# Performance work log

Hardware: AMD Instinct MI355X
Metric: run time of the kernel (lower is better)

The kernel has to match this reference:

```python
import jax, jax.numpy as jnp
import numpy as np

NUM_LAYERS = 2
H = 8        # num_head
D = 64       # dim_head
HID = H * D  # hidden_size = 512
FF = 2048    # dim_ff
SLEN = 256
BSZ = 16
IN_DIM = 512


def setup_inputs() -> dict:
    key = jax.random.key(0)
    ks = jax.random.split(key, 12)
    std = 1.0 / np.sqrt(D)
    return {
        'x': jax.random.normal(ks[0], (SLEN, BSZ, IN_DIM), jnp.float32),
        'in_w': jax.random.normal(ks[1], (IN_DIM, HID), jnp.float32) * 0.02,
        'in_b': jnp.zeros((HID,), jnp.float32),
        'Wy': jax.random.normal(ks[2], (NUM_LAYERS, H, D, D), jnp.float32) * std,
        'Wq': jax.random.normal(ks[3], (NUM_LAYERS, H, D, D), jnp.float32) * std,
        'Wk': jax.random.normal(ks[4], (NUM_LAYERS, H, D, D), jnp.float32) * std,
        'wb': jax.random.normal(ks[5], (NUM_LAYERS, H, D, 4), jnp.float32) * std,
        'Wout': jax.random.normal(ks[6], (NUM_LAYERS, HID, HID), jnp.float32) * 0.02,
        'ln_g': jnp.ones((NUM_LAYERS, HID), jnp.float32),
        'ln_b': jnp.zeros((NUM_LAYERS, HID), jnp.float32),
        'ff_w1': jax.random.normal(ks[7], (NUM_LAYERS, HID, FF), jnp.float32) * 0.02,
        'ff_b1': jnp.zeros((NUM_LAYERS, FF), jnp.float32),
        'ff_w2': jax.random.normal(ks[8], (NUM_LAYERS, FF, HID), jnp.float32) * 0.02,
        'ff_b2': jnp.zeros((NUM_LAYERS, HID), jnp.float32),
        'core_state': 0,
    }


def _layer_norm(x, g, b):
    m = jnp.mean(x, axis=-1, keepdims=True)
    v = jnp.mean(jnp.square(x - m), axis=-1, keepdims=True)
    return (x - m) / jnp.sqrt(v + 1e-5) * g + b


def _sr_block(h, Wy0, Wq0, Wk0, wb0, Wout_l):
    # h: [L, B, HID]. Self-referential fast-weight recurrence (self_ref_v0).
    L, B, _ = h.shape
    x = jax.nn.softmax(h.reshape(L, B, H, D), axis=-1)  # [L,B,H,D]
    init = (
        jnp.broadcast_to(Wy0, (B, H, D, D)),
        jnp.broadcast_to(Wq0, (B, H, D, D)),
        jnp.broadcast_to(Wk0, (B, H, D, D)),
        jnp.broadcast_to(wb0, (B, H, D, 4)),
    )

    def step(carry, xt):
        Wy_, Wq_, Wk_, wb_ = carry
        y = jnp.einsum('bhij,bhj->bhi', Wy_, xt)
        q = jax.nn.softmax(jnp.einsum('bhij,bhj->bhi', Wq_, xt), axis=-1)
        k = jax.nn.softmax(jnp.einsum('bhij,bhj->bhi', Wk_, xt), axis=-1)
        beta = jax.nn.sigmoid(jnp.einsum('bhjf,bhj->bhf', wb_, xt))  # [B,H,4]
        d = q - k
        dy = jnp.einsum('bhij,bhj->bhi', Wy_, d)  # W(q) - W(k) by linearity
        dq = jnp.einsum('bhij,bhj->bhi', Wq_, d)
        dk = jnp.einsum('bhij,bhj->bhi', Wk_, d)
        db = jnp.einsum('bhjf,bhj->bhf', wb_, d)  # [B,H,4]
        kT = k[..., None, :]  # [B,H,1,D]
        Wy_n = Wy_ + beta[..., 0:1, None] * dy[..., :, None] * kT
        Wq_n = Wq_ + beta[..., 1:2, None] * dq[..., :, None] * kT
        Wk_n = Wk_ + beta[..., 2:3, None] * dk[..., :, None] * kT
        wb_n = wb_ + beta[..., 3][..., None, None] * k[..., :, None] * db[..., None, :]
        return (Wy_n, Wq_n, Wk_n, wb_n), y

    _, ys = jax.lax.scan(step, init, x)            # ys: [L,B,H,D]
    out = ys.reshape(L, B, H * D) @ Wout_l          # out_linear (no bias)
    return h + out


def reference(x, in_w, in_b, Wy, Wq, Wk, wb, Wout, ln_g, ln_b,
              ff_w1, ff_b1, ff_w2, ff_b2, core_state):
    out = x @ in_w + in_b  # input_proj
    for i in range(NUM_LAYERS):
        out = _sr_block(out, Wy[i], Wq[i], Wk[i], wb[i], Wout[i])
        y = _layer_norm(out, ln_g[i], ln_b[i])
        out = out + (jax.nn.relu(y @ ff_w1[i] + ff_b1[i]) @ ff_w2[i] + ff_b2[i])
    return out
```

## Files before the change

kernel.cpp:

```cpp
#include <hip/hip_runtime.h>
#include <hip/hip_bf16.h>
#include <math.h>

#define SLEN 256
#define BSZ  16
#define NH   8
#define HD   64
#define HID  512
#define FFD  2048
#define MROWS (SLEN*BSZ)

typedef __attribute__((ext_vector_type(8))) short short8v;
typedef __attribute__((ext_vector_type(4))) float float4v;
typedef unsigned short ushort_t;

#define SYNC_LDS() do { \
  asm volatile("s_waitcnt lgkmcnt(0)" ::: "memory"); \
  __builtin_amdgcn_s_barrier(); \
} while (0)

template<int C> __device__ __forceinline__ float dppf(float x){
  return __int_as_float(__builtin_amdgcn_update_dpp(__float_as_int(x), __float_as_int(x), C, 0xF, 0xF, false));
}

__device__ __forceinline__ float rsum64(float v){
  v += dppf<0xB1>(v);
  v += dppf<0x4E>(v);
  v += dppf<0x141>(v);
  v += dppf<0x140>(v);
  v += __int_as_float(__builtin_amdgcn_update_dpp(0, __float_as_int(v), 0x142, 0xa, 0xF, false));
  v += __int_as_float(__builtin_amdgcn_update_dpp(0, __float_as_int(v), 0x143, 0xc, 0xF, false));
  return __int_as_float(__builtin_amdgcn_readlane(__float_as_int(v), 63));
}

__device__ __forceinline__ float rmax64(float v){
  v = fmaxf(v, dppf<0xB1>(v));
  v = fmaxf(v, dppf<0x4E>(v));
  v = fmaxf(v, dppf<0x141>(v));
  v = fmaxf(v, dppf<0x140>(v));
  v = fmaxf(v, __int_as_float(__builtin_amdgcn_update_dpp((int)0xff800000u, __float_as_int(v), 0x142, 0xa, 0xF, false)));
  v = fmaxf(v, __int_as_float(__builtin_amdgcn_update_dpp((int)0xff800000u, __float_as_int(v), 0x143, 0xc, 0xF, false)));
  return __int_as_float(__builtin_amdgcn_readlane(__float_as_int(v), 63));
}

__device__ __forceinline__ void split_bf16(float f, ushort_t& h, ushort_t& l){
  unsigned u = __float_as_uint(f);
  unsigned r = u + (0x7fffu + ((u >> 16) & 1u));
  h = (ushort_t)(r >> 16);
  float hf = __uint_as_float(((unsigned)h) << 16);
  float lo = f - hf;
  unsigned u2 = __float_as_uint(lo);
  unsigned r2 = u2 + (0x7fffu + ((u2 >> 16) & 1u));
  l = (ushort_t)(r2 >> 16);
}

template<int N, int K, bool BIAS, bool RESID, bool RELU>
__global__ __launch_bounds__(512) void gemm_mfma(
    const float* __restrict__ A, const float* __restrict__ B,
    const float* __restrict__ bias, const float* __restrict__ resid,
    float* __restrict__ C)
{
  __shared__ ushort_t Ah[128][40];
  __shared__ ushort_t Al[128][40];
  __shared__ ushort_t Bh[128][40];
  __shared__ ushort_t Bl[128][40];

  const int tid = threadIdx.x;
  const int wv = tid >> 6, lane = tid & 63;
  const int wm = wv >> 2, wn = wv & 3;
  const int l15 = lane & 15, l16 = lane >> 4;
  const int row0 = blockIdx.y * 128, col0 = blockIdx.x * 128;

  const int sar = tid >> 2, sak = (tid & 3) * 8;
  const int sbc = tid & 127, sbk = (tid >> 7) * 8;

  float4v acc[4][2];
#pragma unroll
  for (int i = 0; i < 4; ++i)
#pragma unroll
    for (int n = 0; n < 2; ++n) acc[i][n] = (float4v)(0.f);

  for (int k0 = 0; k0 < K; k0 += 32) {
    {
      const float* ap = &A[(size_t)(row0 + sar) * K + k0 + sak];
      float4 a0 = *reinterpret_cast<const float4*>(ap);
      float4 a1 = *reinterpret_cast<const float4*>(ap + 4);
      float av[8] = {a0.x, a0.y, a0.z, a0.w, a1.x, a1.y, a1.z, a1.w};
      short8v vh, vl;
#pragma unroll
      for (int j = 0; j < 8; ++j) {
        ushort_t h, l; split_bf16(av[j], h, l);
        vh[j] = (short)h; vl[j] = (short)l;
      }
      *reinterpret_cast<short8v*>(&Ah[sar][sak]) = vh;
      *reinterpret_cast<short8v*>(&Al[sar][sak]) = vl;
    }
    {
      float bv[8];
#pragma unroll
      for (int j = 0; j < 8; ++j)
        bv[j] = B[(size_t)(k0 + sbk + j) * N + col0 + sbc];
      short8v vh, vl;
#pragma unroll
      for (int j = 0; j < 8; ++j) {
        ushort_t h, l; split_bf16(bv[j], h, l);
        vh[j] = (short)h; vl[j] = (short)l;
      }
      *reinterpret_cast<short8v*>(&Bh[sbc][sbk]) = vh;
      *reinterpret_cast<short8v*>(&Bl[sbc][sbk]) = vl;
    }
    __syncthreads();

    short8v ah[4], al[4], bh[2], bl[2];
#pragma unroll
    for (int i = 0; i < 4; ++i) {
      const int r = wm * 64 + i * 16 + l15;
      ah[i] = *reinterpret_cast<const short8v*>(&Ah[r][l16 * 8]);
      al[i] = *reinterpret_cast<const short8v*>(&Al[r][l16 * 8]);
    }
#pragma unroll
    for (int n = 0; n < 2; ++n) {
      const int c = wn * 32 + n * 16 + l15;
      bh[n] = *reinterpret_cast<const short8v*>(&Bh[c][l16 * 8]);
      bl[n] = *reinterpret_cast<const short8v*>(&Bl[c][l16 * 8]);
    }
#pragma unroll
    for (int i = 0; i < 4; ++i)
#pragma unroll
      for (int n = 0; n < 2; ++n) {
        acc[i][n] = __builtin_amdgcn_mfma_f32_16x16x32_bf16(ah[i], bh[n], acc[i][n], 0, 0, 0);
        acc[i][n] = __builtin_amdgcn_mfma_f32_16x16x32_bf16(ah[i], bl[n], acc[i][n], 0, 0, 0);
        acc[i][n] = __builtin_amdgcn_mfma_f32_16x16x32_bf16(al[i], bh[n], acc[i][n], 0, 0, 0);
      }
    __syncthreads();
  }

#pragma unroll
  for (int i = 0; i < 4; ++i) {
#pragma unroll
    for (int n = 0; n < 2; ++n) {
      const int col = col0 + wn * 32 + n * 16 + l15;
      float bs = BIAS ? bias[col] : 0.f;
#pragma unroll
      for (int r = 0; r < 4; ++r) {
        const int row = row0 + wm * 64 + i * 16 + l16 * 4 + r;
        float v = acc[i][n][r] + bs;
        if (RESID) v += resid[(size_t)row * N + col];
        if (RELU)  v = fmaxf(v, 0.f);
        C[(size_t)row * N + col] = v;
      }
    }
  }
}

__global__ __launch_bounds__(64) void layernorm_k(
    const float* __restrict__ in, const float* __restrict__ g,
    const float* __restrict__ b, float* __restrict__ out)
{
  const int row = blockIdx.x, lane = threadIdx.x;
  const float* p = in + (size_t)row * HID + lane * 8;
  float4 v0 = *reinterpret_cast<const float4*>(p);
  float4 v1 = *reinterpret_cast<const float4*>(p + 4);
  float s = v0.x + v0.y + v0.z + v0.w + v1.x + v1.y + v1.z + v1.w;
  s = rsum64(s);
  const float mean = s * (1.0f / HID);
  float x[8] = {v0.x, v0.y, v0.z, v0.w, v1.x, v1.y, v1.z, v1.w};
  float sq = 0.f;
#pragma unroll
  for (int j = 0; j < 8; ++j) { float d = x[j] - mean; sq += d * d; }
  sq = rsum64(sq);
  const float rstd = rsqrtf(sq * (1.0f / HID) + 1e-5f);
  float4 g0 = *reinterpret_cast<const float4*>(&g[lane * 8]);
  float4 g1 = *reinterpret_cast<const float4*>(&g[lane * 8 + 4]);
  float4 b0 = *reinterpret_cast<const float4*>(&b[lane * 8]);
  float4 b1 = *reinterpret_cast<const float4*>(&b[lane * 8 + 4]);
  float gg[8] = {g0.x, g0.y, g0.z, g0.w, g1.x, g1.y, g1.z, g1.w};
  float bb[8] = {b0.x, b0.y, b0.z, b0.w, b1.x, b1.y, b1.z, b1.w};
  float o[8];
#pragma unroll
  for (int j = 0; j < 8; ++j) o[j] = (x[j] - mean) * rstd * gg[j] + bb[j];
  float4 o0 = make_float4(o[0], o[1], o[2], o[3]);
  float4 o1 = make_float4(o[4], o[5], o[6], o[7]);
  float* q = out + (size_t)row * HID + lane * 8;
  *reinterpret_cast<float4*>(q) = o0;
  *reinterpret_cast<float4*>(q + 4) = o1;
}

__global__ __launch_bounds__(256) void srec4(
    const float* __restrict__ h,
    const float* __restrict__ Wy0, const float* __restrict__ Wq0,
    const float* __restrict__ Wk0, const float* __restrict__ wb0,
    float* __restrict__ ys)
{
  const int bh = blockIdx.x;
  const int bb = bh >> 3, hh = bh & 7;
  const int tid = threadIdx.x;
  const int wv = tid >> 6, lane = tid & 63;

  __shared__ float xs[2][64];
  __shared__ float q_s[2][64];
  __shared__ float k_s[2][64];
  __shared__ float4 betas4[2];

  float W[64];
  float wbr[4] = {0.f, 0.f, 0.f, 0.f};
  float xrA = 0.f, xrB = 0.f;
  float xnreg = 0.f;

  const float* xp = h + (size_t)bb * HID + hh * 64 + lane;
  float* yp = ys + (size_t)bb * HID + hh * 64 + lane;

  if (wv < 3) {
    const float* base = (wv == 0 ? Wy0 : (wv == 1 ? Wq0 : Wk0)) + (size_t)(hh * 64 + lane) * 64;
#pragma unroll
    for (int j = 0; j < 16; ++j) {
      float4 a = reinterpret_cast<const float4*>(base)[j];
      W[4*j] = a.x; W[4*j+1] = a.y; W[4*j+2] = a.z; W[4*j+3] = a.w;
    }
  } else {
    float4 w = *reinterpret_cast<const float4*>(&wb0[(size_t)(hh * 64 + lane) * 4]);
    wbr[0] = w.x; wbr[1] = w.y; wbr[2] = w.z; wbr[3] = w.w;
    float xr0 = xp[0];
    xrA = xp[(size_t)BSZ * HID];
    float m = rmax64(xr0);
    float e = __expf(xr0 - m);
    float sm = rsum64(e);
    float x0 = e * __builtin_amdgcn_rcpf(sm);
    xs[0][lane] = x0;
    float s0 = rsum64(wbr[0] * x0);
    float s1 = rsum64(wbr[1] * x0);
    float s2 = rsum64(wbr[2] * x0);
    float s3 = rsum64(wbr[3] * x0);
    if (lane == 0)
      betas4[0] = make_float4(1.f / (1.f + __expf(-s0)), 1.f / (1.f + __expf(-s1)),
                              1.f / (1.f + __expf(-s2)), 1.f / (1.f + __expf(-s3)));
  }
  SYNC_LDS();

  auto stepf = [&](int P, float& XCUR, float& XNEXT, int T) {
    if (wv == 3) {
      if (T + 2 < SLEN) XNEXT = xp[(size_t)(T + 2) * BSZ * HID];
      float m = rmax64(XCUR);
      float e = __expf(XCUR - m);
      float sm = rsum64(e);
      float xn_ = e * __builtin_amdgcn_rcpf(sm);
      xs[1 - P][lane] = xn_;
      xnreg = xn_;
    } else {
      const float4* xv = reinterpret_cast<const float4*>(xs[P]);
      float a0 = 0.f, a1 = 0.f, a2 = 0.f, a3 = 0.f;
#pragma unroll
      for (int j = 0; j < 16; ++j) {
        float4 xx = xv[j];
        a0 = fmaf(W[4*j],   xx.x, a0);
        a1 = fmaf(W[4*j+1], xx.y, a1);
        a2 = fmaf(W[4*j+2], xx.z, a2);
        a3 = fmaf(W[4*j+3], xx.w, a3);
      }
      float acc = (a0 + a1) + (a2 + a3);
      if (wv == 0) {
        yp[(size_t)T * BSZ * HID] = acc;
      } else {
        float m = rmax64(acc);
        float e = __expf(acc - m);
        float sm = rsum64(e);
        float v = e * __builtin_amdgcn_rcpf(sm);
        float* dst = (wv == 1) ? q_s[P] : k_s[P];
        dst[lane] = v;
      }
    }

    SYNC_LDS();

    float4 bb4 = betas4[P];
    if (wv < 3) {
      const float4* qv = reinterpret_cast<const float4*>(q_s[P]);
      const float4* kv = reinterpret_cast<const float4*>(k_s[P]);
      float a0 = 0.f, a1 = 0.f, a2 = 0.f, a3 = 0.f;
#pragma unroll
      for (int j = 0; j < 16; ++j) {
        float4 q4 = qv[j], k4 = kv[j];
        a0 = fmaf(W[4*j],   q4.x - k4.x, a0);
        a1 = fmaf(W[4*j+1], q4.y - k4.y, a1);
        a2 = fmaf(W[4*j+2], q4.z - k4.z, a2);
        a3 = fmaf(W[4*j+3], q4.w - k4.w, a3);
      }
      float dd = (a0 + a1) + (a2 + a3);
      float beta = (wv == 0) ? bb4.x : (wv == 1 ? bb4.y : bb4.z);
      float c = beta * dd;
#pragma unroll
      for (int j = 0; j < 16; ++j) {
        float4 k4 = kv[j];
        W[4*j]   = fmaf(c, k4.x, W[4*j]);
        W[4*j+1] = fmaf(c, k4.y, W[4*j+1]);
        W[4*j+2] = fmaf(c, k4.z, W[4*j+2]);
        W[4*j+3] = fmaf(c, k4.w, W[4*j+3]);
      }
    } else {
      float ql = q_s[P][lane], kl = k_s[P][lane];
      float dl = ql - kl;
      float d0 = rsum64(wbr[0] * dl);
      float d1 = rsum64(wbr[1] * dl);
      float d2 = rsum64(wbr[2] * dl);
      float d3 = rsum64(wbr[3] * dl);
      float bk = bb4.w * kl;
      wbr[0] = fmaf(bk, d0, wbr[0]);
      wbr[1] = fmaf(bk, d1, wbr[1]);
      wbr[2] = fmaf(bk, d2, wbr[2]);
      wbr[3] = fmaf(bk, d3, wbr[3]);
      float s0 = rsum64(wbr[0] * xnreg);
      float s1 = rsum64(wbr[1] * xnreg);
      float s2 = rsum64(wbr[2] * xnreg);
      float s3 = rsum64(wbr[3] * xnreg);
      if (lane == 0)
        betas4[1 - P] = make_float4(1.f / (1.f + __expf(-s0)), 1.f / (1.f + __expf(-s1)),
                                    1.f / (1.f + __expf(-s2)), 1.f / (1.f + __expf(-s3)));
    }
  };

  for (int t = 0; t < SLEN; t += 2) {
    stepf(0, xrA, xrB, t);
    stepf(1, xrB, xrA, t + 1);
  }
}

extern "C" void kernel_launch(void* const* d_in, const int* in_sizes, int n_in,
                              void* d_out, int out_size, void* d_ws, size_t ws_size,
                              hipStream_t stream)
{
  const float* x     = (const float*)d_in[0];
  const float* in_w  = (const float*)d_in[1];
  const float* in_b  = (const float*)d_in[2];
  const float* Wy    = (const float*)d_in[3];
  const float* Wq    = (const float*)d_in[4];
  const float* Wk    = (const float*)d_in[5];
  const float* wb    = (const float*)d_in[6];
  const float* Wout  = (const float*)d_in[7];
  const float* ln_g  = (const float*)d_in[8];
  const float* ln_b  = (const float*)d_in[9];
  const float* ff_w1 = (const float*)d_in[10];
  const float* ff_b1 = (const float*)d_in[11];
  const float* ff_w2 = (const float*)d_in[12];
  const float* ff_b2 = (const float*)d_in[13];
  float* out = (float*)d_out;

  char* ws = (char*)d_ws;
  float* ys   = (float*)ws;
  float* ffb  = (float*)(ws + (8u << 20));
  float* ybuf = (float*)(ws + (40u << 20));

  gemm_mfma<HID, 512, true, false, false><<<dim3(HID/128, MROWS/128), 512, 0, stream>>>(
      x, in_w, in_b, nullptr, out);

  for (int l = 0; l < 2; ++l) {
    srec4<<<128, 256, 0, stream>>>(out,
                                   Wy + (size_t)l * NH * HD * HD,
                                   Wq + (size_t)l * NH * HD * HD,
                                   Wk + (size_t)l * NH * HD * HD,
                                   wb + (size_t)l * NH * HD * 4,
                                   ys);
    gemm_mfma<HID, HID, false, true, false><<<dim3(HID/128, MROWS/128), 512, 0, stream>>>(
        ys, Wout + (size_t)l * HID * HID, nullptr, out, out);
    layernorm_k<<<MROWS, 64, 0, stream>>>(out, ln_g + (size_t)l * HID, ln_b + (size_t)l * HID, ybuf);
    gemm_mfma<FFD, HID, true, false, true><<<dim3(FFD/128, MROWS/128), 512, 0, stream>>>(
        ybuf, ff_w1 + (size_t)l * HID * FFD, ff_b1 + (size_t)l * FFD, nullptr, ffb);
    gemm_mfma<HID, FFD, true, true, false><<<dim3(HID/128, MROWS/128), 512, 0, stream>>>(
        ffb, ff_w2 + (size_t)l * FFD * HID, ff_b2 + (size_t)l * HID, out, out);
  }
}
```

Measured before the change: 994.0 us.

## Collapse recurrence into single-wave kernel with precomputed softmax inputs

Replaces the 4-wave per-head recurrence kernel, which synchronised with block barriers twice per timestep, with one 64-lane wave per (batch, head) that holds all three weight matrices in registers. The input softmax moves into a separate parallel kernel that writes a head-major layout. The recurrence kernel streams that layout into LDS in chunks through async global-to-LDS loads. This removes the per-step barriers, but each wave now does three times the FMA work serially and needs about 200 registers. With only 128 waves launched, occupancy is low.

```diff
diff --git a/kernel.cpp b/kernel.cpp
--- a/kernel.cpp
+++ b/kernel.cpp
@@ -13,11 +13,6 @@
 typedef __attribute__((ext_vector_type(8))) short short8v;
 typedef __attribute__((ext_vector_type(4))) float float4v;
 typedef unsigned short ushort_t;
-
-#define SYNC_LDS() do { \
-  asm volatile("s_waitcnt lgkmcnt(0)" ::: "memory"); \
-  __builtin_amdgcn_s_barrier(); \
-} while (0)
 
 template<int C> __device__ __forceinline__ float dppf(float x){
   return __int_as_float(__builtin_amdgcn_update_dpp(__float_as_int(x), __float_as_int(x), C, 0xF, 0xF, false));
@@ -186,141 +181,156 @@
   *reinterpret_cast<float4*>(q + 4) = o1;
 }
 
-__global__ __launch_bounds__(256) void srec4(
-    const float* __restrict__ h,
+__global__ __launch_bounds__(256) void softmax_x(
+    const float* __restrict__ in, float* __restrict__ xs)
+{
+  const int r = blockIdx.x * 4 + (threadIdx.x >> 6);
+  const int lane = threadIdx.x & 63;
+  float v = in[(size_t)r * 64 + lane];
+  float m = rmax64(v);
+  float e = __expf(v - m);
+  float s = rsum64(e);
+  float o = e * __builtin_amdgcn_rcpf(s);
+  const int t = r >> 7;
+  const int b = (r >> 3) & 15;
+  const int h = r & 7;
+  xs[(((size_t)(b * 8 + h)) * SLEN + t) * 64 + lane] = o;
+}
+
+#define CH 32
+#define NCH (SLEN/CH)
+
+__device__ __forceinline__ void stage_chunk(const float* src, float* dst_lds, int lane){
+#pragma unroll
+  for (int i = 0; i < (CH*64)/256; ++i)
+    __builtin_amdgcn_global_load_lds(
+        (const __attribute__((address_space(1))) void*)(src + i*256 + lane*4),
+        (__attribute__((address_space(3))) void*)(dst_lds + i*256), 16, 0, 0);
+}
+
+__global__ __launch_bounds__(64) void srec1w(
+    const float* __restrict__ xs,
     const float* __restrict__ Wy0, const float* __restrict__ Wq0,
     const float* __restrict__ Wk0, const float* __restrict__ wb0,
     float* __restrict__ ys)
 {
   const int bh = blockIdx.x;
   const int bb = bh >> 3, hh = bh & 7;
-  const int tid = threadIdx.x;
-  const int wv = tid >> 6, lane = tid & 63;
-
-  __shared__ float xs[2][64];
-  __shared__ float q_s[2][64];
-  __shared__ float k_s[2][64];
-  __shared__ float4 betas4[2];
-
-  float W[64];
-  float wbr[4] = {0.f, 0.f, 0.f, 0.f};
-  float xrA = 0.f, xrB = 0.f;
-  float xnreg = 0.f;
-
-  const float* xp = h + (size_t)bb * HID + hh * 64 + lane;
+  const int lane = threadIdx.x;
+
+  __shared__ __align__(16) float xls[2][CH*64];
+  __shared__ __align__(16) float dkb[128];
+
+  float Wy[64], Wq[64], Wk[64];
+  float wbr[4];
+  {
+    const float4* py = reinterpret_cast<const float4*>(Wy0 + (size_t)(hh*64 + lane) * 64);
+    const float4* pq = reinterpret_cast<const float4*>(Wq0 + (size_t)(hh*64 + lane) * 64);
+    const float4* pk = reinterpret_cast<const float4*>(Wk0 + (size_t)(hh*64 + lane) * 64);
+#pragma unroll
+    for (int j = 0; j < 16; ++j) {
+      float4 a = py[j]; Wy[4*j]=a.x; Wy[4*j+1]=a.y; Wy[4*j+2]=a.z; Wy[4*j+3]=a.w;
+      float4 b = pq[j]; Wq[4*j]=b.x; Wq[4*j+1]=b.y; Wq[4*j+2]=b.z; Wq[4*j+3]=b.w;
+      float4 c = pk[j]; Wk[4*j]=c.x; Wk[4*j+1]=c.y; Wk[4*j+2]=c.z; Wk[4*j+3]=c.w;
+    }
+    float4 w = *reinterpret_cast<const float4*>(&wb0[(size_t)(hh*64 + lane) * 4]);
+    wbr[0] = w.x; wbr[1] = w.y; wbr[2] = w.z; wbr[3] = w.w;
+  }
+
+  const float* xsb = xs + (size_t)bh * SLEN * 64;
   float* yp = ys + (size_t)bb * HID + hh * 64 + lane;
 
-  if (wv < 3) {
-    const float* base = (wv == 0 ? Wy0 : (wv == 1 ? Wq0 : Wk0)) + (size_t)(hh * 64 + lane) * 64;
-#pragma unroll
-    for (int j = 0; j < 16; ++j) {
-      float4 a = reinterpret_cast<const float4*>(base)[j];
-      W[4*j] = a.x; W[4*j+1] = a.y; W[4*j+2] = a.z; W[4*j+3] = a.w;
-    }
-  } else {
-    float4 w = *reinterpret_cast<const float4*>(&wb0[(size_t)(hh * 64 + lane) * 4]);
-    wbr[0] = w.x; wbr[1] = w.y; wbr[2] = w.z; wbr[3] = w.w;
-    float xr0 = xp[0];
-    xrA = xp[(size_t)BSZ * HID];
-    float m = rmax64(xr0);
-    float e = __expf(xr0 - m);
-    float sm = rsum64(e);
-    float x0 = e * __builtin_amdgcn_rcpf(sm);
-    xs[0][lane] = x0;
-    float s0 = rsum64(wbr[0] * x0);
-    float s1 = rsum64(wbr[1] * x0);
-    float s2 = rsum64(wbr[2] * x0);
-    float s3 = rsum64(wbr[3] * x0);
-    if (lane == 0)
-      betas4[0] = make_float4(1.f / (1.f + __expf(-s0)), 1.f / (1.f + __expf(-s1)),
-                              1.f / (1.f + __expf(-s2)), 1.f / (1.f + __expf(-s3)));
-  }
-  SYNC_LDS();
-
-  auto stepf = [&](int P, float& XCUR, float& XNEXT, int T) {
-    if (wv == 3) {
-      if (T + 2 < SLEN) XNEXT = xp[(size_t)(T + 2) * BSZ * HID];
-      float m = rmax64(XCUR);
-      float e = __expf(XCUR - m);
-      float sm = rsum64(e);
-      float xn_ = e * __builtin_amdgcn_rcpf(sm);
-      xs[1 - P][lane] = xn_;
-      xnreg = xn_;
-    } else {
-      const float4* xv = reinterpret_cast<const float4*>(xs[P]);
-      float a0 = 0.f, a1 = 0.f, a2 = 0.f, a3 = 0.f;
+  stage_chunk(xsb, &xls[0][0], lane);
+  asm volatile("s_waitcnt vmcnt(0)" ::: "memory");
+
+  int buf = 0;
+  for (int c = 0; c < NCH; ++c) {
+    if (c + 1 < NCH) stage_chunk(xsb + (size_t)(c+1)*CH*64, &xls[buf^1][0], lane);
+
+    for (int s = 0; s < CH; ++s) {
+      const int t = c * CH + s;
+
+      float xown = xls[buf][s*64 + lane];
+      float t0 = rsum64(wbr[0] * xown);
+      float t1 = rsum64(wbr[1] * xown);
+      float t2 = rsum64(wbr[2] * xown);
+      float t3 = rsum64(wbr[3] * xown);
+      float beta0 = 1.f / (1.f + __expf(-t0));
+      float beta1 = 1.f / (1.f + __expf(-t1));
+      float beta2 = 1.f / (1.f + __expf(-t2));
+      float beta3 = 1.f / (1.f + __expf(-t3));
+
+      const float4* xv = reinterpret_cast<const float4*>(&xls[buf][s*64]);
+      float ay0=0,ay1=0,ay2=0,ay3=0, aq0=0,aq1=0,aq2=0,aq3=0, ak0=0,ak1=0,ak2=0,ak3=0;
 #pragma unroll
       for (int j = 0; j < 16; ++j) {
-        float4 xx = xv[j];
-        a0 = fmaf(W[4*j],   xx.x, a0);
-        a1 = fmaf(W[4*j+1], xx.y, a1);
-        a2 = fmaf(W[4*j+2], xx.z, a2);
-        a3 = fmaf(W[4*j+3], xx.w, a3);
-      }
-      float acc = (a0 + a1) + (a2 + a3);
-      if (wv == 0) {
-        yp[(size_t)T * BSZ * HID] = acc;
-      } else {
-        float m = rmax64(acc);
-        float e = __expf(acc - m);
-        float sm = rsum64(e);
-        float v = e * __builtin_amdgcn_rcpf(sm);
-        float* dst = (wv == 1) ? q_s[P] : k_s[P];
-        dst[lane] = v;
-      }
-    }
-
-    SYNC_LDS();
-
-    float4 bb4 = betas4[P];
-    if (wv < 3) {
-      const float4* qv = reinterpret_cast<const float4*>(q_s[P]);
-      const float4* kv = reinterpret_cast<const float4*>(k_s[P]);
-      float a0 = 0.f, a1 = 0.f, a2 = 0.f, a3 = 0.f;
+        float4 x4 = xv[j];
+        ay0 = fmaf(Wy[4*j],   x4.x, ay0); ay1 = fmaf(Wy[4*j+1], x4.y, ay1);
+        ay2 = fmaf(Wy[4*j+2], x4.z, ay2); ay3 = fmaf(Wy[4*j+3], x4.w, ay3);
+        aq0 = fmaf(Wq[4*j],   x4.x, aq0); aq1 = fmaf(Wq[4*j+1], x4.y, aq1);
+        aq2 = fmaf(Wq[4*j+2], x4.z, aq2); aq3 = fmaf(Wq[4*j+3], x4.w, aq3);
+        ak0 = fmaf(Wk[4*j],   x4.x, ak0); ak1 = fmaf(Wk[4*j+1], x4.y, ak1);
+        ak2 = fmaf(Wk[4*j+2], x4.z, ak2); ak3 = fmaf(Wk[4*j+3], x4.w, ak3);
+      }
+      float ay = (ay0+ay1)+(ay2+ay3);
+      float aq = (aq0+aq1)+(aq2+aq3);
+      float ak = (ak0+ak1)+(ak2+ak3);
+
+      yp[(size_t)t * BSZ * HID] = ay;
+
+      float mq = rmax64(aq); float eq = __expf(aq - mq); float sq = rsum64(eq);
+      float q_l = eq * __builtin_amdgcn_rcpf(sq);
+      float mk = rmax64(ak); float ek = __expf(ak - mk); float sk = rsum64(ek);
+      float k_l = ek * __builtin_amdgcn_rcpf(sk);
+      float d_l = q_l - k_l;
+
+      dkb[lane]      = d_l;
+      dkb[64 + lane] = k_l;
+
+      float e0 = rsum64(wbr[0] * d_l);
+      float e1 = rsum64(wbr[1] * d_l);
+      float e2 = rsum64(wbr[2] * d_l);
+      float e3 = rsum64(wbr[3] * d_l);
+      float bk = beta3 * k_l;
+      wbr[0] = fmaf(bk, e0, wbr[0]);
+      wbr[1] = fmaf(bk, e1, wbr[1]);
+      wbr[2] = fmaf(bk, e2, wbr[2]);
+      wbr[3] = fmaf(bk, e3, wbr[3]);
+
+      const float4* dv = reinterpret_cast<const float4*>(&dkb[0]);
+      const float4* kv = reinterpret_cast<const float4*>(&dkb[64]);
+      float4 karr[16];
+      float dy0=0,dy1=0,dy2=0,dy3=0, dq0=0,dq1=0,dq2=0,dq3=0, dk0=0,dk1=0,dk2=0,dk3=0;
 #pragma unroll
       for (int j = 0; j < 16; ++j) {
-        float4 q4 = qv[j], k4 = kv[j];
-        a0 = fmaf(W[4*j],   q4.x - k4.x, a0);
-        a1 = fmaf(W[4*j+1], q4.y - k4.y, a1);
-        a2 = fmaf(W[4*j+2], q4.z - k4.z, a2);
-        a3 = fmaf(W[4*j+3], q4.w - k4.w, a3);
-      }
-      float dd = (a0 + a1) + (a2 + a3);
-      float beta = (wv == 0) ? bb4.x : (wv == 1 ? bb4.y : bb4.z);
-      float c = beta * dd;
+        float4 d4 = dv[j];
+        float4 k4 = kv[j];
+        karr[j] = k4;
+        dy0 = fmaf(Wy[4*j],   d4.x, dy0); dy1 = fmaf(Wy[4*j+1], d4.y, dy1);
+        dy2 = fmaf(Wy[4*j+2], d4.z, dy2); dy3 = fmaf(Wy[4*j+3], d4.w, dy3);
+        dq0 = fmaf(Wq[4*j],   d4.x, dq0); dq1 = fmaf(Wq[4*j+1], d4.y, dq1);
+        dq2 = fmaf(Wq[4*j+2], d4.z, dq2); dq3 = fmaf(Wq[4*j+3], d4.w, dq3);
+        dk0 = fmaf(Wk[4*j],   d4.x, dk0); dk1 = fmaf(Wk[4*j+1], d4.y, dk1);
+        dk2 = fmaf(Wk[4*j+2], d4.z, dk2); dk3 = fmaf(Wk[4*j+3], d4.w, dk3);
+      }
+      float dy = (dy0+dy1)+(dy2+dy3);
+      float dq = (dq0+dq1)+(dq2+dq3);
+      float dk = (dk0+dk1)+(dk2+dk3);
+      float cy = beta0 * dy, cq = beta1 * dq, ck = beta2 * dk;
 #pragma unroll
       for (int j = 0; j < 16; ++j) {
-        float4 k4 = kv[j];
-        W[4*j]   = fmaf(c, k4.x, W[4*j]);
-        W[4*j+1] = fmaf(c, k4.y, W[4*j+1]);
-        W[4*j+2] = fmaf(c, k4.z, W[4*j+2]);
-        W[4*j+3] = fmaf(c, k4.w, W[4*j+3]);
-      }
-    } else {
-      float ql = q_s[P][lane], kl = k_s[P][lane];
-      float dl = ql - kl;
-      float d0 = rsum64(wbr[0] * dl);
-      float d1 = rsum64(wbr[1] * dl);
-      float d2 = rsum64(wbr[2] * dl);
-      float d3 = rsum64(wbr[3] * dl);
-      float bk = bb4.w * kl;
-      wbr[0] = fmaf(bk, d0, wbr[0]);
-      wbr[1] = fmaf(bk, d1, wbr[1]);
-      wbr[2] = fmaf(bk, d2, wbr[2]);
-      wbr[3] = fmaf(bk, d3, wbr[3]);
-      float s0 = rsum64(wbr[0] * xnreg);
-      float s1 = rsum64(wbr[1] * xnreg);
-      float s2 = rsum64(wbr[2] * xnreg);
-      float s3 = rsum64(wbr[3] * xnreg);
-      if (lane == 0)
-        betas4[1 - P] = make_float4(1.f / (1.f + __expf(-s0)), 1.f / (1.f + __expf(-s1)),
-                                    1.f / (1.f + __expf(-s2)), 1.f / (1.f + __expf(-s3)));
-    }
-  };
-
-  for (int t = 0; t < SLEN; t += 2) {
-    stepf(0, xrA, xrB, t);
-    stepf(1, xrB, xrA, t + 1);
+        float4 k4 = karr[j];
+        Wy[4*j]   = fmaf(cy, k4.x, Wy[4*j]);   Wy[4*j+1] = fmaf(cy, k4.y, Wy[4*j+1]);
+        Wy[4*j+2] = fmaf(cy, k4.z, Wy[4*j+2]); Wy[4*j+3] = fmaf(cy, k4.w, Wy[4*j+3]);
+        Wq[4*j]   = fmaf(cq, k4.x, Wq[4*j]);   Wq[4*j+1] = fmaf(cq, k4.y, Wq[4*j+1]);
+        Wq[4*j+2] = fmaf(cq, k4.z, Wq[4*j+2]); Wq[4*j+3] = fmaf(cq, k4.w, Wq[4*j+3]);
+        Wk[4*j]   = fmaf(ck, k4.x, Wk[4*j]);   Wk[4*j+1] = fmaf(ck, k4.y, Wk[4*j+1]);
+        Wk[4*j+2] = fmaf(ck, k4.z, Wk[4*j+2]); Wk[4*j+3] = fmaf(ck, k4.w, Wk[4*j+3]);
+      }
+    }
+
+    asm volatile("s_waitcnt vmcnt(0)" ::: "memory");
+    buf ^= 1;
   }
 }
 
@@ -348,12 +358,14 @@
   float* ys   = (float*)ws;
   float* ffb  = (float*)(ws + (8u << 20));
   float* ybuf = (float*)(ws + (40u << 20));
+  float* xsb  = ybuf;
 
   gemm_mfma<HID, 512, true, false, false><<<dim3(HID/128, MROWS/128), 512, 0, stream>>>(
       x, in_w, in_b, nullptr, out);
 
   for (int l = 0; l < 2; ++l) {
-    srec4<<<128, 256, 0, stream>>>(out,
+    softmax_x<<<(SLEN*BSZ*NH)/4, 256, 0, stream>>>(out, xsb);
+    srec1w<<<128, 64, 0, stream>>>(xsb,
                                    Wy + (size_t)l * NH * HD * HD,
                                    Wq + (size_t)l * NH * HD * HD,
                                    Wk + (size_t)l * NH * HD * HD,
```

Result: slower. 1.771 ms (+78.2%).

## Precompute next-step W·x with old weights and correct via rank-1 update

Applied to the files above, without the earlier changes.

The recurrent kernel now computes W·x_{t+1} in the same loop as W·(q−k), using the pre-update weights, so that pass is off the critical path. At the next step the output is fixed up with the rank-1 term beta·dd·(k·x_next), where the dot k·x_next comes from the wb warp through LDS. This takes a dependent 64-FMA pass out of the serial chain. In exchange it adds a second barrier per step and extra registers for the cached k values.

```diff
diff --git a/kernel.cpp b/kernel.cpp
--- a/kernel.cpp
+++ b/kernel.cpp
@@ -186,7 +186,7 @@
   *reinterpret_cast<float4*>(q + 4) = o1;
 }
 
-__global__ __launch_bounds__(256) void srec4(
+__global__ __launch_bounds__(256) void srec4s(
     const float* __restrict__ h,
     const float* __restrict__ Wy0, const float* __restrict__ Wq0,
     const float* __restrict__ Wk0, const float* __restrict__ wb0,
@@ -201,11 +201,15 @@
   __shared__ float q_s[2][64];
   __shared__ float k_s[2][64];
   __shared__ float4 betas4[2];
+  __shared__ float gdot[2];
 
   float W[64];
   float wbr[4] = {0.f, 0.f, 0.f, 0.f};
   float xrA = 0.f, xrB = 0.f;
   float xnreg = 0.f;
+  float shadow = 0.f;
+  float v_prev = 0.f;
+  float c_prev = 0.f;
 
   const float* xp = h + (size_t)bb * HID + hh * 64 + lane;
   float* yp = ys + (size_t)bb * HID + hh * 64 + lane;
@@ -231,11 +235,27 @@
     float s1 = rsum64(wbr[1] * x0);
     float s2 = rsum64(wbr[2] * x0);
     float s3 = rsum64(wbr[3] * x0);
-    if (lane == 0)
+    if (lane == 0) {
       betas4[0] = make_float4(1.f / (1.f + __expf(-s0)), 1.f / (1.f + __expf(-s1)),
                               1.f / (1.f + __expf(-s2)), 1.f / (1.f + __expf(-s3)));
+      gdot[0] = 0.f; gdot[1] = 0.f;
+    }
   }
   SYNC_LDS();
+
+  if (wv < 3) {
+    const float4* xv = reinterpret_cast<const float4*>(xs[0]);
+    float s0 = 0.f, s1 = 0.f, s2 = 0.f, s3 = 0.f;
+#pragma unroll
+    for (int j = 0; j < 16; ++j) {
+      float4 x4 = xv[j];
+      s0 = fmaf(W[4*j],   x4.x, s0);
+      s1 = fmaf(W[4*j+1], x4.y, s1);
+      s2 = fmaf(W[4*j+2], x4.z, s2);
+      s3 = fmaf(W[4*j+3], x4.w, s3);
+    }
+    shadow = (s0 + s1) + (s2 + s3);
+  }
 
   auto stepf = [&](int P, float& XCUR, float& XNEXT, int T) {
     if (wv == 3) {
@@ -247,17 +267,7 @@
       xs[1 - P][lane] = xn_;
       xnreg = xn_;
     } else {
-      const float4* xv = reinterpret_cast<const float4*>(xs[P]);
-      float a0 = 0.f, a1 = 0.f, a2 = 0.f, a3 = 0.f;
-#pragma unroll
-      for (int j = 0; j < 16; ++j) {
-        float4 xx = xv[j];
-        a0 = fmaf(W[4*j],   xx.x, a0);
-        a1 = fmaf(W[4*j+1], xx.y, a1);
-        a2 = fmaf(W[4*j+2], xx.z, a2);
-        a3 = fmaf(W[4*j+3], xx.w, a3);
-      }
-      float acc = (a0 + a1) + (a2 + a3);
+      float acc = fmaf(c_prev * gdot[P], v_prev, shadow);
       if (wv == 0) {
         yp[(size_t)T * BSZ * HID] = acc;
       } else {
@@ -276,26 +286,37 @@
     if (wv < 3) {
       const float4* qv = reinterpret_cast<const float4*>(q_s[P]);
       const float4* kv = reinterpret_cast<const float4*>(k_s[P]);
+      const float4* xv = reinterpret_cast<const float4*>(xs[1 - P]);
+      float4 karr[16];
       float a0 = 0.f, a1 = 0.f, a2 = 0.f, a3 = 0.f;
+      float s0 = 0.f, s1 = 0.f, s2 = 0.f, s3 = 0.f;
 #pragma unroll
       for (int j = 0; j < 16; ++j) {
-        float4 q4 = qv[j], k4 = kv[j];
+        float4 q4 = qv[j], k4 = kv[j], x4 = xv[j];
+        karr[j] = k4;
         a0 = fmaf(W[4*j],   q4.x - k4.x, a0);
         a1 = fmaf(W[4*j+1], q4.y - k4.y, a1);
         a2 = fmaf(W[4*j+2], q4.z - k4.z, a2);
         a3 = fmaf(W[4*j+3], q4.w - k4.w, a3);
+        s0 = fmaf(W[4*j],   x4.x, s0);
+        s1 = fmaf(W[4*j+1], x4.y, s1);
+        s2 = fmaf(W[4*j+2], x4.z, s2);
+        s3 = fmaf(W[4*j+3], x4.w, s3);
       }
       float dd = (a0 + a1) + (a2 + a3);
+      shadow = (s0 + s1) + (s2 + s3);
       float beta = (wv == 0) ? bb4.x : (wv == 1 ? bb4.y : bb4.z);
       float c = beta * dd;
 #pragma unroll
       for (int j = 0; j < 16; ++j) {
-        float4 k4 = kv[j];
+        float4 k4 = karr[j];
         W[4*j]   = fmaf(c, k4.x, W[4*j]);
         W[4*j+1] = fmaf(c, k4.y, W[4*j+1]);
         W[4*j+2] = fmaf(c, k4.z, W[4*j+2]);
         W[4*j+3] = fmaf(c, k4.w, W[4*j+3]);
       }
+      v_prev = dd;
+      c_prev = beta;
     } else {
       float ql = q_s[P][lane], kl = k_s[P][lane];
       float dl = ql - kl;
@@ -303,6 +324,7 @@
       float d1 = rsum64(wbr[1] * dl);
       float d2 = rsum64(wbr[2] * dl);
       float d3 = rsum64(wbr[3] * dl);
+      float g  = rsum64(kl * xnreg);
       float bk = bb4.w * kl;
       wbr[0] = fmaf(bk, d0, wbr[0]);
       wbr[1] = fmaf(bk, d1, wbr[1]);
@@ -312,10 +334,14 @@
       float s1 = rsum64(wbr[1] * xnreg);
       float s2 = rsum64(wbr[2] * xnreg);
       float s3 = rsum64(wbr[3] * xnreg);
-      if (lane == 0)
+      if (lane == 0) {
         betas4[1 - P] = make_float4(1.f / (1.f + __expf(-s0)), 1.f / (1.f + __expf(-s1)),
                                     1.f / (1.f + __expf(-s2)), 1.f / (1.f + __expf(-s3)));
-    }
+        gdot[1 - P] = g;
+      }
+    }
+
+    SYNC_LDS();
   };
 
   for (int t = 0; t < SLEN; t += 2) {
@@ -353,12 +379,12 @@
       x, in_w, in_b, nullptr, out);
 
   for (int l = 0; l < 2; ++l) {
-    srec4<<<128, 256, 0, stream>>>(out,
-                                   Wy + (size_t)l * NH * HD * HD,
-                                   Wq + (size_t)l * NH * HD * HD,
-                                   Wk + (size_t)l * NH * HD * HD,
-                                   wb + (size_t)l * NH * HD * 4,
-                                   ys);
+    srec4s<<<128, 256, 0, stream>>>(out,
+                                    Wy + (size_t)l * NH * HD * HD,
+                                    Wq + (size_t)l * NH * HD * HD,
+                                    Wk + (size_t)l * NH * HD * HD,
+                                    wb + (size_t)l * NH * HD * 4,
+                                    ys);
     gemm_mfma<HID, HID, false, true, false><<<dim3(HID/128, MROWS/128), 512, 0, stream>>>(
         ys, Wout + (size_t)l * HID * HID, nullptr, out, out);
     layernorm_k<<<MROWS, 64, 0, stream>>>(out, ln_g + (size_t)l * HID, ln_b + (size_t)l * HID, ybuf);
```

After: 1.103 ms. +11.0%, slower.

## Shorten recurrence critical path: skip softmax max, algebraic beta, more ILP

Applied to the files above, without the earlier changes.

In the self-referential recurrence kernel, the beta logits for the next step are now computed from the pre-update fast weights plus a rank-1 correction. This lets those reductions run alongside the update reductions instead of after them. The softmax max-subtraction reductions are dropped, which relies on the logits being small enough that exp cannot overflow. The dot products use eight accumulators, k is kept in registers for the outer-product update instead of being reloaded from LDS, and the sigmoid uses a fast reciprocal. These changes target the serial chain of wave reductions in each timestep, at the cost of some numerical robustness.

```diff
diff --git a/kernel.cpp b/kernel.cpp
--- a/kernel.cpp
+++ b/kernel.cpp
@@ -30,16 +30,6 @@
   v += dppf<0x140>(v);
   v += __int_as_float(__builtin_amdgcn_update_dpp(0, __float_as_int(v), 0x142, 0xa, 0xF, false));
   v += __int_as_float(__builtin_amdgcn_update_dpp(0, __float_as_int(v), 0x143, 0xc, 0xF, false));
-  return __int_as_float(__builtin_amdgcn_readlane(__float_as_int(v), 63));
-}
-
-__device__ __forceinline__ float rmax64(float v){
-  v = fmaxf(v, dppf<0xB1>(v));
-  v = fmaxf(v, dppf<0x4E>(v));
-  v = fmaxf(v, dppf<0x141>(v));
-  v = fmaxf(v, dppf<0x140>(v));
-  v = fmaxf(v, __int_as_float(__builtin_amdgcn_update_dpp((int)0xff800000u, __float_as_int(v), 0x142, 0xa, 0xF, false)));
-  v = fmaxf(v, __int_as_float(__builtin_amdgcn_update_dpp((int)0xff800000u, __float_as_int(v), 0x143, 0xc, 0xF, false)));
   return __int_as_float(__builtin_amdgcn_readlane(__float_as_int(v), 63));
 }
 
@@ -186,7 +176,7 @@
   *reinterpret_cast<float4*>(q + 4) = o1;
 }
 
-__global__ __launch_bounds__(256) void srec4(
+__global__ __launch_bounds__(256) void srec4t(
     const float* __restrict__ h,
     const float* __restrict__ Wy0, const float* __restrict__ Wq0,
     const float* __restrict__ Wk0, const float* __restrict__ wb0,
@@ -222,8 +212,7 @@
     wbr[0] = w.x; wbr[1] = w.y; wbr[2] = w.z; wbr[3] = w.w;
     float xr0 = xp[0];
     xrA = xp[(size_t)BSZ * HID];
-    float m = rmax64(xr0);
-    float e = __expf(xr0 - m);
+    float e = __expf(xr0);
     float sm = rsum64(e);
     float x0 = e * __builtin_amdgcn_rcpf(sm);
     xs[0][lane] = x0;
@@ -232,37 +221,41 @@
     float s2 = rsum64(wbr[2] * x0);
     float s3 = rsum64(wbr[3] * x0);
     if (lane == 0)
-      betas4[0] = make_float4(1.f / (1.f + __expf(-s0)), 1.f / (1.f + __expf(-s1)),
-                              1.f / (1.f + __expf(-s2)), 1.f / (1.f + __expf(-s3)));
+      betas4[0] = make_float4(__builtin_amdgcn_rcpf(1.f + __expf(-s0)),
+                              __builtin_amdgcn_rcpf(1.f + __expf(-s1)),
+                              __builtin_amdgcn_rcpf(1.f + __expf(-s2)),
+                              __builtin_amdgcn_rcpf(1.f + __expf(-s3)));
   }
   SYNC_LDS();
 
   auto stepf = [&](int P, float& XCUR, float& XNEXT, int T) {
     if (wv == 3) {
       if (T + 2 < SLEN) XNEXT = xp[(size_t)(T + 2) * BSZ * HID];
-      float m = rmax64(XCUR);
-      float e = __expf(XCUR - m);
+      float e = __expf(XCUR);
       float sm = rsum64(e);
       float xn_ = e * __builtin_amdgcn_rcpf(sm);
       xs[1 - P][lane] = xn_;
       xnreg = xn_;
     } else {
       const float4* xv = reinterpret_cast<const float4*>(xs[P]);
-      float a0 = 0.f, a1 = 0.f, a2 = 0.f, a3 = 0.f;
-#pragma unroll
-      for (int j = 0; j < 16; ++j) {
-        float4 xx = xv[j];
-        a0 = fmaf(W[4*j],   xx.x, a0);
-        a1 = fmaf(W[4*j+1], xx.y, a1);
-        a2 = fmaf(W[4*j+2], xx.z, a2);
-        a3 = fmaf(W[4*j+3], xx.w, a3);
-      }
-      float acc = (a0 + a1) + (a2 + a3);
+      float a0=0.f,a1=0.f,a2=0.f,a3=0.f,a4=0.f,a5=0.f,a6=0.f,a7=0.f;
+#pragma unroll
+      for (int j = 0; j < 8; ++j) {
+        float4 x1 = xv[2*j], x2 = xv[2*j+1];
+        a0 = fmaf(W[8*j+0], x1.x, a0);
+        a1 = fmaf(W[8*j+1], x1.y, a1);
+        a2 = fmaf(W[8*j+2], x1.z, a2);
+        a3 = fmaf(W[8*j+3], x1.w, a3);
+        a4 = fmaf(W[8*j+4], x2.x, a4);
+        a5 = fmaf(W[8*j+5], x2.y, a5);
+        a6 = fmaf(W[8*j+6], x2.z, a6);
+        a7 = fmaf(W[8*j+7], x2.w, a7);
+      }
+      float acc = ((a0 + a1) + (a2 + a3)) + ((a4 + a5) + (a6 + a7));
       if (wv == 0) {
         yp[(size_t)T * BSZ * HID] = acc;
       } else {
-        float m = rmax64(acc);
-        float e = __expf(acc - m);
+        float e = __expf(acc);
         float sm = rsum64(e);
         float v = e * __builtin_amdgcn_rcpf(sm);
         float* dst = (wv == 1) ? q_s[P] : k_s[P];
@@ -276,21 +269,28 @@
     if (wv < 3) {
       const float4* qv = reinterpret_cast<const float4*>(q_s[P]);
       const float4* kv = reinterpret_cast<const float4*>(k_s[P]);
-      float a0 = 0.f, a1 = 0.f, a2 = 0.f, a3 = 0.f;
-#pragma unroll
-      for (int j = 0; j < 16; ++j) {
-        float4 q4 = qv[j], k4 = kv[j];
-        a0 = fmaf(W[4*j],   q4.x - k4.x, a0);
-        a1 = fmaf(W[4*j+1], q4.y - k4.y, a1);
-        a2 = fmaf(W[4*j+2], q4.z - k4.z, a2);
-        a3 = fmaf(W[4*j+3], q4.w - k4.w, a3);
-      }
-      float dd = (a0 + a1) + (a2 + a3);
+      float4 karr[16];
+      float a0=0.f,a1=0.f,a2=0.f,a3=0.f,a4=0.f,a5=0.f,a6=0.f,a7=0.f;
+#pragma unroll
+      for (int j = 0; j < 8; ++j) {
+        float4 q1 = qv[2*j], k1 = kv[2*j];
+        float4 q2 = qv[2*j+1], k2 = kv[2*j+1];
+        karr[2*j] = k1; karr[2*j+1] = k2;
+        a0 = fmaf(W[8*j+0], q1.x - k1.x, a0);
+        a1 = fmaf(W[8*j+1], q1.y - k1.y, a1);
+        a2 = fmaf(W[8*j+2], q1.z - k1.z, a2);
+        a3 = fmaf(W[8*j+3], q1.w - k1.w, a3);
+        a4 = fmaf(W[8*j+4], q2.x - k2.x, a4);
+        a5 = fmaf(W[8*j+5], q2.y - k2.y, a5);
+        a6 = fmaf(W[8*j+6], q2.z - k2.z, a6);
+        a7 = fmaf(W[8*j+7], q2.w - k2.w, a7);
+      }
+      float dd = ((a0 + a1) + (a2 + a3)) + ((a4 + a5) + (a6 + a7));
       float beta = (wv == 0) ? bb4.x : (wv == 1 ? bb4.y : bb4.z);
       float c = beta * dd;
 #pragma unroll
       for (int j = 0; j < 16; ++j) {
-        float4 k4 = kv[j];
+        float4 k4 = karr[j];
         W[4*j]   = fmaf(c, k4.x, W[4*j]);
         W[4*j+1] = fmaf(c, k4.y, W[4*j+1]);
         W[4*j+2] = fmaf(c, k4.z, W[4*j+2]);
@@ -299,22 +299,29 @@
     } else {
       float ql = q_s[P][lane], kl = k_s[P][lane];
       float dl = ql - kl;
+      float bk = bb4.w * kl;
+      float u0 = rsum64(wbr[0] * xnreg);
+      float u1 = rsum64(wbr[1] * xnreg);
+      float u2 = rsum64(wbr[2] * xnreg);
+      float u3 = rsum64(wbr[3] * xnreg);
       float d0 = rsum64(wbr[0] * dl);
       float d1 = rsum64(wbr[1] * dl);
       float d2 = rsum64(wbr[2] * dl);
       float d3 = rsum64(wbr[3] * dl);
-      float bk = bb4.w * kl;
+      float g  = rsum64(bk * xnreg);
       wbr[0] = fmaf(bk, d0, wbr[0]);
       wbr[1] = fmaf(bk, d1, wbr[1]);
       wbr[2] = fmaf(bk, d2, wbr[2]);
       wbr[3] = fmaf(bk, d3, wbr[3]);
-      float s0 = rsum64(wbr[0] * xnreg);
-      float s1 = rsum64(wbr[1] * xnreg);
-      float s2 = rsum64(wbr[2] * xnreg);
-      float s3 = rsum64(wbr[3] * xnreg);
+      float s0 = fmaf(d0, g, u0);
+      float s1 = fmaf(d1, g, u1);
+      float s2 = fmaf(d2, g, u2);
+      float s3 = fmaf(d3, g, u3);
       if (lane == 0)
-        betas4[1 - P] = make_float4(1.f / (1.f + __expf(-s0)), 1.f / (1.f + __expf(-s1)),
-                                    1.f / (1.f + __expf(-s2)), 1.f / (1.f + __expf(-s3)));
+        betas4[1 - P] = make_float4(__builtin_amdgcn_rcpf(1.f + __expf(-s0)),
+                                    __builtin_amdgcn_rcpf(1.f + __expf(-s1)),
+                                    __builtin_amdgcn_rcpf(1.f + __expf(-s2)),
+                                    __builtin_amdgcn_rcpf(1.f + __expf(-s3)));
     }
   };
 
@@ -353,12 +360,12 @@
       x, in_w, in_b, nullptr, out);
 
   for (int l = 0; l < 2; ++l) {
-    srec4<<<128, 256, 0, stream>>>(out,
-                                   Wy + (size_t)l * NH * HD * HD,
-                                   Wq + (size_t)l * NH * HD * HD,
-                                   Wk + (size_t)l * NH * HD * HD,
-                                   wb + (size_t)l * NH * HD * 4,
-                                   ys);
+    srec4t<<<128, 256, 0, stream>>>(out,
+                                    Wy + (size_t)l * NH * HD * HD,
+                                    Wq + (size_t)l * NH * HD * HD,
+                                    Wk + (size_t)l * NH * HD * HD,
+                                    wb + (size_t)l * NH * HD * 4,
+                                    ys);
     gemm_mfma<HID, HID, false, true, false><<<dim3(HID/128, MROWS/128), 512, 0, stream>>>(
         ys, Wout + (size_t)l * HID * HID, nullptr, out, out);
     layernorm_k<<<MROWS, 64, 0, stream>>>(out, ln_g + (size_t)l * HID, ln_b + (size_t)l * HID, ybuf);
```

After: 943.9 us. 5.0% less time.
